# Performance work log

Measured on AMD Instinct MI355X. Metric: run time of the kernel, lower is better.

The kernel has to match this reference:

```python
import jax, jax.numpy as jnp
import numpy as np

B, S, D, H = 2, 2048, 1024, 16
DK = D // H


def setup_inputs() -> dict:
    key = jax.random.key(0)
    ks = jax.random.split(key, 11)
    s = 1.0 / np.sqrt(D)
    inp = {
        "q": jax.random.normal(ks[0], (B, S, D), jnp.float32),
        "k": jax.random.normal(ks[1], (B, S, D), jnp.float32),
        "v": jax.random.normal(ks[2], (B, S, D), jnp.float32),
        # causal (lower-triangular) decoder mask, broadcast over batch & heads
        "mask": jnp.tril(jnp.ones((S, S), jnp.int32))[None, None, :, :],
        "Wq": jax.random.normal(ks[3], (D, D), jnp.float32) * s,
        "bq": jax.random.normal(ks[4], (D,), jnp.float32) * s,
        "Wk": jax.random.normal(ks[5], (D, D), jnp.float32) * s,
        "bk": jax.random.normal(ks[6], (D,), jnp.float32) * s,
        "Wv": jax.random.normal(ks[7], (D, D), jnp.float32) * s,
        "bv": jax.random.normal(ks[8], (D,), jnp.float32) * s,
        "Wo": jax.random.normal(ks[9], (D, D), jnp.float32) * s,
        "bo": jax.random.normal(ks[10], (D,), jnp.float32) * s,
    }
    return inp


def reference(q, k, v, mask, Wq, bq, Wk, bk, Wv, bv, Wo, bo):
    # projections (nn.Linear: x @ W.T + b)
    def proj(x, W, b):
        return (x @ W.T + b).reshape(B, S, H, DK).transpose(0, 2, 1, 3)  # [B,H,S,DK]

    Q = proj(q, Wq, bq)
    K = proj(k, Wk, bk)
    V = proj(v, Wv, bv)

    scores = jnp.einsum("bhsd,bhtd->bhst", Q, K) / jnp.sqrt(jnp.float32(DK))
    scores = jnp.where(mask == 0, jnp.float32(-1e9), scores)
    attn = jax.nn.softmax(scores, axis=-1)  # dropout=0.0 -> identity
    ctx = jnp.einsum("bhst,bhtd->bhsd", attn, V)
    ctx = ctx.transpose(0, 2, 1, 3).reshape(B, S, D)
    return ctx @ Wo.T + bo
```

## Files before the change

### kernel.cpp

```cpp
#include <hip/hip_runtime.h>

typedef __bf16 bf16;
typedef __bf16 bf16x4 __attribute__((ext_vector_type(4)));
typedef __bf16 bf16x8 __attribute__((ext_vector_type(8)));
typedef float floatx4 __attribute__((ext_vector_type(4)));

#define NB 2
#define NS 2048
#define ND 1024
#define NH 16
#define NDK 64
#define NM (NB * NS)

__device__ __forceinline__ void async_cp16(const void* g, void* l) {
  __builtin_amdgcn_global_load_lds(
      (const __attribute__((address_space(1))) void*)g,
      (__attribute__((address_space(3))) void*)l, 16, 0, 0);
}

__device__ __forceinline__ bf16x8 cvt8(const float* p) {
  float4 lo = *(const float4*)p, hi = *(const float4*)(p + 4);
  bf16x8 o;
  o[0] = (bf16)lo.x; o[1] = (bf16)lo.y; o[2] = (bf16)lo.z; o[3] = (bf16)lo.w;
  o[4] = (bf16)hi.x; o[5] = (bf16)hi.y; o[6] = (bf16)hi.z; o[7] = (bf16)hi.w;
  return o;
}

__device__ __forceinline__ void wg_barrier_lds() {
  __asm__ __volatile__("s_waitcnt lgkmcnt(0)" ::: "memory");
  __builtin_amdgcn_s_barrier();
}

__device__ __forceinline__ void tr2(const void* p, bf16x4& lo, bf16x4& hi) {
  asm volatile("ds_read_b64_tr_b16 %0, %2\n\t"
               "ds_read_b64_tr_b16 %1, %2 offset:512"
               : "=&v"(lo), "=&v"(hi)
               : "v"((const __attribute__((address_space(3))) void*)p));
}

__device__ __forceinline__ float fexp2(float x) {
  float r;
  asm("v_exp_f32 %0, %1" : "=v"(r) : "v"(x));
  return r;
}

struct CvtArgs {
  const float* src[8];
  bf16* dst[8];
  int nblk[8];
  int nseg;
};

__global__ __launch_bounds__(256) void cvt_kernel(CvtArgs a) {
  int b = blockIdx.x, seg = 0;
  while (seg < a.nseg - 1 && b >= a.nblk[seg]) { b -= a.nblk[seg]; ++seg; }
  const size_t idx = ((size_t)b * 256 + threadIdx.x) * 8;
  *(bf16x8*)(a.dst[seg] + idx) = cvt8(a.src[seg] + idx);
}

template <int TM, typename TA, typename TC>
__global__ __launch_bounds__(256) void gemm_dma(
    const TA* __restrict__ A0, const TA* __restrict__ A1, const TA* __restrict__ A2,
    const bf16* __restrict__ W0, const bf16* __restrict__ W1, const bf16* __restrict__ W2,
    const float* __restrict__ bias0, const float* __restrict__ bias1, const float* __restrict__ bias2,
    TC* __restrict__ C0, TC* __restrict__ C1, TC* __restrict__ C2)
{
  const int z = blockIdx.z;
  const TA* A = (z == 0) ? A0 : (z == 1) ? A1 : A2;
  const bf16* W = (z == 0) ? W0 : (z == 1) ? W1 : W2;
  const float* bias = (z == 0) ? bias0 : (z == 1) ? bias1 : bias2;
  TC* C = (z == 0) ? C0 : (z == 1) ? C1 : C2;

  __shared__ bf16 At[TM * 32];
  __shared__ bf16 Bt[128 * 32];

  const int tid = threadIdx.x;
  const int wave = tid >> 6, lane = tid & 63;
  const int q4 = lane >> 4, l15 = lane & 15;
  const int m0 = blockIdx.y * TM, n0 = blockIdx.x * 128;
  constexpr int WM = TM / 2;
  constexpr int MI = WM / 16;
  const int wm = (wave >> 1) * WM, wn = (wave & 1) * 64;

  floatx4 acc[MI][4] = {};

  const bf16* Wg = W + (size_t)(n0 + (lane >> 2)) * ND + (lane & 3) * 8;
  const bf16* Ag = nullptr;
  const float* Af = nullptr;
  const int srow = tid >> 2, sk = (tid & 3) * 8;
  if constexpr (sizeof(TA) == 2)
    Ag = (const bf16*)A + (size_t)(m0 + (lane >> 2)) * ND + (lane & 3) * 8;
  else
    Af = (const float*)A + (size_t)(m0 + srow) * ND + sk;

  for (int k0 = 0; k0 < ND; k0 += 32) {
    bf16x8 a0, a1;
    if constexpr (sizeof(TA) == 4) {
      a0 = cvt8(Af + k0);
      if constexpr (TM == 128) a1 = cvt8(Af + (size_t)64 * ND + k0);
    }
    __syncthreads();
#pragma unroll
    for (int c2 = 0; c2 < 2; ++c2) {
      const int c = wave * 2 + c2;
      async_cp16(Wg + (size_t)c * 16 * ND + k0, &Bt[c * 16 * 32]);
    }
    if constexpr (sizeof(TA) == 2) {
#pragma unroll
      for (int c2 = 0; c2 < TM / 64; ++c2) {
        const int c = wave * (TM / 64) + c2;
        async_cp16(Ag + (size_t)c * 16 * ND + k0, &At[c * 16 * 32]);
      }
    } else {
      *(bf16x8*)&At[srow * 32 + sk] = a0;
      if constexpr (TM == 128) *(bf16x8*)&At[(srow + 64) * 32 + sk] = a1;
    }
    __syncthreads();

    bf16x8 af[MI], bfr[4];
#pragma unroll
    for (int i = 0; i < MI; ++i)
      af[i] = *(const bf16x8*)&At[(wm + i * 16 + l15) * 32 + q4 * 8];
#pragma unroll
    for (int j = 0; j < 4; ++j)
      bfr[j] = *(const bf16x8*)&Bt[(wn + j * 16 + l15) * 32 + q4 * 8];
#pragma unroll
    for (int i = 0; i < MI; ++i)
#pragma unroll
      for (int j = 0; j < 4; ++j)
        acc[i][j] = __builtin_amdgcn_mfma_f32_16x16x32_bf16(af[i], bfr[j], acc[i][j], 0, 0, 0);
  }

#pragma unroll
  for (int j = 0; j < 4; ++j) {
    const int col = n0 + wn + j * 16 + l15;
    const float bv = bias[col];
#pragma unroll
    for (int i = 0; i < MI; ++i) {
      const int rowb = m0 + wm + i * 16 + q4 * 4;
#pragma unroll
      for (int r = 0; r < 4; ++r)
        C[(size_t)(rowb + r) * ND + col] = (TC)(acc[i][j][r] + bv);
    }
  }
}

#define NEGBIG (-1e30f)
#define LDP 72

__global__ __launch_bounds__(256) void attn_kernel(
    const bf16* __restrict__ Q, const bf16* __restrict__ K,
    const bf16* __restrict__ V, bf16* __restrict__ O)
{
  __shared__ bf16 vt[2][4096];
  __shared__ bf16 pbuf[4][16 * LDP];

  const int bx = blockIdx.x;
  const int h = blockIdx.y, b = blockIdx.z;
  const int tid = threadIdx.x, wave = tid >> 6, lane = tid & 63;
  const int q4 = lane >> 4, l15 = lane & 15;

  const int koff = l15 * ND + q4 * 8;
  const int sg0 = wave * 8 + (lane >> 3);
  const int sg1 = 32 + sg0;
  const int vs0 = ((sg0 >> 2) << 2) + ((lane & 7) >> 1);
  const int vs1 = ((sg1 >> 2) << 2) + ((lane & 7) >> 1);
  const int vd0 = (sg0 & 3) * 16 + (lane & 1) * 8;
  const int vd1 = (sg1 & 3) * 16 + (lane & 1) * 8;
  const int voff0 = vs0 * ND + vd0;
  const int voff1 = vs1 * ND + vd1;

  const int trb = (lane >> 4) * 512 + l15 * 4;

  bf16x8 qf[2];
  floatx4 oacc[4];
  float psum[4];
  bf16x8 kA[8], kB[8];

  auto ldK = [&](int j, bf16x8 (&kk)[8]) {
    const bf16* ub = K + ((size_t)(b * NS + j * 64)) * ND + h * NDK;
#pragma unroll
    for (int nf = 0; nf < 4; ++nf)
#pragma unroll
      for (int t = 0; t < 2; ++t)
        kk[nf * 2 + t] = *(const bf16x8*)(ub + koff + nf * 16 * ND + t * 32);
  };
  auto stageV = [&](int j, int buf) {
    const bf16* ub = V + ((size_t)(b * NS + j * 64)) * ND + h * NDK;
    async_cp16(ub + voff0, &vt[buf][wave * 512]);
    async_cp16(ub + voff1, &vt[buf][2048 + wave * 512]);
  };

  auto body = [&](int j, int iq, bf16x8 (&kc)[8], bf16x8 (&kn)[8]) {
    const int cur = j & 1;

    floatx4 sf[4];
    __builtin_amdgcn_s_setprio(1);
#pragma unroll
    for (int nf = 0; nf < 4; ++nf) {
      floatx4 s = {0.f, 0.f, 0.f, 0.f};
      s = __builtin_amdgcn_mfma_f32_16x16x32_bf16(qf[0], kc[nf * 2 + 0], s, 0, 0, 0);
      s = __builtin_amdgcn_mfma_f32_16x16x32_bf16(qf[1], kc[nf * 2 + 1], s, 0, 0, 0);
      sf[nf] = s;
    }
    __builtin_amdgcn_s_setprio(0);

    wg_barrier_lds();

    if (j < iq) {
      stageV(j + 1, cur ^ 1);
      asm volatile("" ::: "memory");
      ldK(j + 1, kn);
    }

    if (j == iq) {
#pragma unroll
      for (int nf = 0; nf < 4; ++nf) {
        const int kc2 = nf * 16 + l15;
#pragma unroll
        for (int r = 0; r < 4; ++r)
          if (kc2 > wave * 16 + q4 * 4 + r) sf[nf][r] = NEGBIG;
      }
    }

    bf16x4 vlo[4][2], vhi[4][2];
#pragma unroll
    for (int nf = 0; nf < 4; ++nf)
#pragma unroll
      for (int t = 0; t < 2; ++t)
        tr2(&vt[cur][t * 2048 + nf * 64 + trb], vlo[nf][t], vhi[nf][t]);

#pragma unroll
    for (int nf = 0; nf < 4; ++nf)
#pragma unroll
      for (int r = 0; r < 4; ++r) {
        const float pv = fexp2(sf[nf][r]);
        psum[r] += pv;
        pbuf[wave][(q4 * 4 + r) * LDP + nf * 16 + l15] = (bf16)pv;
      }

    asm volatile("s_waitcnt lgkmcnt(0)" ::: "memory");
    __builtin_amdgcn_sched_barrier(0);

    bf16x8 pa0 = *(const bf16x8*)&pbuf[wave][l15 * LDP + q4 * 8];
    bf16x8 pa1 = *(const bf16x8*)&pbuf[wave][l15 * LDP + 32 + q4 * 8];

    __builtin_amdgcn_s_setprio(1);
#pragma unroll
    for (int nf = 0; nf < 4; ++nf) {
      bf16x8 vb0 = __builtin_shufflevector(vlo[nf][0], vhi[nf][0], 0, 1, 2, 3, 4, 5, 6, 7);
      bf16x8 vb1 = __builtin_shufflevector(vlo[nf][1], vhi[nf][1], 0, 1, 2, 3, 4, 5, 6, 7);
      oacc[nf] = __builtin_amdgcn_mfma_f32_16x16x32_bf16(pa0, vb0, oacc[nf], 0, 0, 0);
      oacc[nf] = __builtin_amdgcn_mfma_f32_16x16x32_bf16(pa1, vb1, oacc[nf], 0, 0, 0);
    }
    __builtin_amdgcn_s_setprio(0);
  };

  for (int ph = 0; ph < 2; ++ph) {
    const int iq = ph ? (31 - bx) : bx;
    __syncthreads();

    const size_t qrow0 = (size_t)(b * NS + iq * 64 + wave * 16 + l15);
#pragma unroll
    for (int t = 0; t < 2; ++t) {
      bf16x8 tmp = *(const bf16x8*)(Q + qrow0 * ND + h * NDK + t * 32 + q4 * 8);
#pragma unroll
      for (int e = 0; e < 8; ++e) qf[t][e] = (bf16)((float)tmp[e] * 0.180336880f);
    }

#pragma unroll
    for (int nf = 0; nf < 4; ++nf) oacc[nf] = floatx4{0.f, 0.f, 0.f, 0.f};
#pragma unroll
    for (int r = 0; r < 4; ++r) psum[r] = 0.f;

    stageV(0, 0);
    asm volatile("" ::: "memory");
    ldK(0, kA);
    for (int j = 0; j <= iq; ++j) {
      if ((j & 1) == 0) body(j, iq, kA, kB);
      else              body(j, iq, kB, kA);
    }

#pragma unroll
    for (int r = 0; r < 4; ++r)
#pragma unroll
      for (int off = 1; off < 16; off <<= 1) psum[r] += __shfl_xor(psum[r], off, 16);

#pragma unroll
    for (int nf = 0; nf < 4; ++nf)
#pragma unroll
      for (int r = 0; r < 4; ++r) {
        const int qrow = iq * 64 + wave * 16 + q4 * 4 + r;
        O[(size_t)(b * NS + qrow) * ND + h * NDK + nf * 16 + l15] =
            (bf16)(oacc[nf][r] / psum[r]);
      }
  }
}

extern "C" void kernel_launch(void* const* d_in, const int* in_sizes, int n_in,
                              void* d_out, int out_size, void* d_ws, size_t ws_size,
                              hipStream_t stream) {
  const float* q  = (const float*)d_in[0];
  const float* k  = (const float*)d_in[1];
  const float* v  = (const float*)d_in[2];
  const float* Wq = (const float*)d_in[4];
  const float* bq = (const float*)d_in[5];
  const float* Wk = (const float*)d_in[6];
  const float* bk = (const float*)d_in[7];
  const float* Wv = (const float*)d_in[8];
  const float* bv = (const float*)d_in[9];
  const float* Wo = (const float*)d_in[10];
  const float* bo = (const float*)d_in[11];
  float* out = (float*)d_out;
  char* w = (char*)d_ws;

  const dim3 attn_grid(NS / 128, NH, NB);

  if (ws_size >= (size_t)56 << 20) {
    bf16* xq = (bf16*)(w);
    bf16* xk = (bf16*)(w + ((size_t)8 << 20));
    bf16* xv = (bf16*)(w + ((size_t)16 << 20));
    bf16* wq = (bf16*)(w + ((size_t)24 << 20));
    bf16* wk = (bf16*)(w + ((size_t)26 << 20));
    bf16* wv = (bf16*)(w + ((size_t)28 << 20));
    bf16* wo = (bf16*)(w + ((size_t)30 << 20));
    bf16* Qb = (bf16*)(w + ((size_t)32 << 20));
    bf16* Kb = (bf16*)(w + ((size_t)40 << 20));
    bf16* Vb = (bf16*)(w + ((size_t)48 << 20));
    bf16* Ob = xq;

    CvtArgs ca{};
    const int b4 = (int)((size_t)NM * ND / 2048);
    const int b1 = (int)((size_t)ND * ND / 2048);
    ca.src[0] = q;  ca.dst[0] = xq; ca.nblk[0] = b4;
    ca.src[1] = k;  ca.dst[1] = xk; ca.nblk[1] = b4;
    ca.src[2] = v;  ca.dst[2] = xv; ca.nblk[2] = b4;
    ca.src[3] = Wq; ca.dst[3] = wq; ca.nblk[3] = b1;
    ca.src[4] = Wk; ca.dst[4] = wk; ca.nblk[4] = b1;
    ca.src[5] = Wv; ca.dst[5] = wv; ca.nblk[5] = b1;
    ca.src[6] = Wo; ca.dst[6] = wo; ca.nblk[6] = b1;
    ca.nseg = 7;
    cvt_kernel<<<3 * b4 + 4 * b1, 256, 0, stream>>>(ca);

    gemm_dma<128, bf16, bf16><<<dim3(8, 32, 3), 256, 0, stream>>>(
        xq, xk, xv, wq, wk, wv, bq, bk, bv, Qb, Kb, Vb);
    attn_kernel<<<attn_grid, 256, 0, stream>>>(Qb, Kb, Vb, Ob);
    gemm_dma<64, bf16, float><<<dim3(8, 64, 1), 256, 0, stream>>>(
        Ob, Ob, Ob, wo, wo, wo, bo, bo, bo, out, out, out);
  } else if (ws_size >= (size_t)40 << 20) {
    bf16* wq = (bf16*)(w);
    bf16* wk = (bf16*)(w + ((size_t)2 << 20));
    bf16* wv = (bf16*)(w + ((size_t)4 << 20));
    bf16* wo = (bf16*)(w + ((size_t)6 << 20));
    bf16* Qb = (bf16*)(w + ((size_t)8 << 20));
    bf16* Kb = (bf16*)(w + ((size_t)16 << 20));
    bf16* Vb = (bf16*)(w + ((size_t)24 << 20));
    bf16* Ob = (bf16*)(w + ((size_t)32 << 20));

    CvtArgs ca{};
    const int b1 = (int)((size_t)ND * ND / 2048);
    ca.src[0] = Wq; ca.dst[0] = wq; ca.nblk[0] = b1;
    ca.src[1] = Wk; ca.dst[1] = wk; ca.nblk[1] = b1;
    ca.src[2] = Wv; ca.dst[2] = wv; ca.nblk[2] = b1;
    ca.src[3] = Wo; ca.dst[3] = wo; ca.nblk[3] = b1;
    ca.nseg = 4;
    cvt_kernel<<<4 * b1, 256, 0, stream>>>(ca);

    gemm_dma<128, float, bf16><<<dim3(8, 32, 3), 256, 0, stream>>>(
        q, k, v, wq, wk, wv, bq, bk, bv, Qb, Kb, Vb);
    attn_kernel<<<attn_grid, 256, 0, stream>>>(Qb, Kb, Vb, Ob);
    gemm_dma<64, bf16, float><<<dim3(8, 64, 1), 256, 0, stream>>>(
        Ob, Ob, Ob, wo, wo, wo, bo, bo, bo, out, out, out);
  }
}
```

Measured before the change: 259.6 us.

## Stage K through swizzled LDS with a triple-buffered async K/V pipeline

K tiles are now loaded with async global-to-LDS copies into an XOR-swizzled shared buffer instead of directly into registers. Both K and V move to a three-stage ring buffer that prefetches two tiles ahead, with a vmcnt wait and a barrier at the top of each iteration. The goal is to hide global load latency better and free the registers that held the double-buffered K fragments. The cost is extra LDS (about 48 KB more), which may lower occupancy, plus an extra LDS read of K on every iteration.

```diff
diff --git a/kernel.cpp b/kernel.cpp
--- a/kernel.cpp
+++ b/kernel.cpp
@@ -24,11 +24,6 @@
   o[0] = (bf16)lo.x; o[1] = (bf16)lo.y; o[2] = (bf16)lo.z; o[3] = (bf16)lo.w;
   o[4] = (bf16)hi.x; o[5] = (bf16)hi.y; o[6] = (bf16)hi.z; o[7] = (bf16)hi.w;
   return o;
-}
-
-__device__ __forceinline__ void wg_barrier_lds() {
-  __asm__ __volatile__("s_waitcnt lgkmcnt(0)" ::: "memory");
-  __builtin_amdgcn_s_barrier();
 }
 
 __device__ __forceinline__ void tr2(const void* p, bf16x4& lo, bf16x4& hi) {
@@ -152,7 +147,8 @@
     const bf16* __restrict__ Q, const bf16* __restrict__ K,
     const bf16* __restrict__ V, bf16* __restrict__ O)
 {
-  __shared__ bf16 vt[2][4096];
+  __shared__ bf16 kt[3][4096];
+  __shared__ bf16 vt[3][4096];
   __shared__ bf16 pbuf[4][16 * LDP];
 
   const int bx = blockIdx.x;
@@ -160,7 +156,9 @@
   const int tid = threadIdx.x, wave = tid >> 6, lane = tid & 63;
   const int q4 = lane >> 4, l15 = lane & 15;
 
-  const int koff = l15 * ND + q4 * 8;
+  const int ksrc = (lane >> 3) * ND + 8 * ((lane & 7) ^ ((lane >> 3) & 7));
+  const int kro0 = l15 * 64 + ((q4 + 0) ^ (l15 & 7)) * 8;
+  const int kro1 = l15 * 64 + ((q4 + 4) ^ (l15 & 7)) * 8;
   const int sg0 = wave * 8 + (lane >> 3);
   const int sg1 = 32 + sg0;
   const int vs0 = ((sg0 >> 2) << 2) + ((lane & 7) >> 1);
@@ -169,30 +167,38 @@
   const int vd1 = (sg1 & 3) * 16 + (lane & 1) * 8;
   const int voff0 = vs0 * ND + vd0;
   const int voff1 = vs1 * ND + vd1;
-
   const int trb = (lane >> 4) * 512 + l15 * 4;
 
   bf16x8 qf[2];
   floatx4 oacc[4];
   float psum[4];
-  bf16x8 kA[8], kB[8];
-
-  auto ldK = [&](int j, bf16x8 (&kk)[8]) {
-    const bf16* ub = K + ((size_t)(b * NS + j * 64)) * ND + h * NDK;
-#pragma unroll
-    for (int nf = 0; nf < 4; ++nf)
-#pragma unroll
-      for (int t = 0; t < 2; ++t)
-        kk[nf * 2 + t] = *(const bf16x8*)(ub + koff + nf * 16 * ND + t * 32);
+
+  auto stage = [&](int j, int buf) {
+    const bf16* ubK = K + ((size_t)(b * NS + j * 64)) * ND + h * NDK;
+    const bf16* ubV = V + ((size_t)(b * NS + j * 64)) * ND + h * NDK;
+#pragma unroll
+    for (int c2 = 0; c2 < 2; ++c2) {
+      const int c = wave * 2 + c2;
+      async_cp16(ubK + c * 8 * ND + ksrc, &kt[buf][c * 512]);
+    }
+    async_cp16(ubV + voff0, &vt[buf][wave * 512]);
+    async_cp16(ubV + voff1, &vt[buf][2048 + wave * 512]);
   };
-  auto stageV = [&](int j, int buf) {
-    const bf16* ub = V + ((size_t)(b * NS + j * 64)) * ND + h * NDK;
-    async_cp16(ub + voff0, &vt[buf][wave * 512]);
-    async_cp16(ub + voff1, &vt[buf][2048 + wave * 512]);
-  };
-
-  auto body = [&](int j, int iq, bf16x8 (&kc)[8], bf16x8 (&kn)[8]) {
-    const int cur = j & 1;
+
+  auto body = [&](int j, int iq, int cur, int tgt) {
+    if (j < iq) asm volatile("s_waitcnt vmcnt(4)" ::: "memory");
+    else        asm volatile("s_waitcnt vmcnt(0)" ::: "memory");
+    __builtin_amdgcn_s_barrier();
+    asm volatile("" ::: "memory");
+
+    if (j + 2 <= iq) stage(j + 2, tgt);
+
+    bf16x8 kc[8];
+#pragma unroll
+    for (int nf = 0; nf < 4; ++nf) {
+      kc[nf * 2 + 0] = *(const bf16x8*)&kt[cur][nf * 1024 + kro0];
+      kc[nf * 2 + 1] = *(const bf16x8*)&kt[cur][nf * 1024 + kro1];
+    }
 
     floatx4 sf[4];
     __builtin_amdgcn_s_setprio(1);
@@ -205,14 +211,6 @@
     }
     __builtin_amdgcn_s_setprio(0);
 
-    wg_barrier_lds();
-
-    if (j < iq) {
-      stageV(j + 1, cur ^ 1);
-      asm volatile("" ::: "memory");
-      ldK(j + 1, kn);
-    }
-
     if (j == iq) {
 #pragma unroll
       for (int nf = 0; nf < 4; ++nf) {
@@ -273,12 +271,13 @@
 #pragma unroll
     for (int r = 0; r < 4; ++r) psum[r] = 0.f;
 
-    stageV(0, 0);
-    asm volatile("" ::: "memory");
-    ldK(0, kA);
+    stage(0, 0);
+    if (iq >= 1) stage(1, 1);
+
+    int jm = 0;
     for (int j = 0; j <= iq; ++j) {
-      if ((j & 1) == 0) body(j, iq, kA, kB);
-      else              body(j, iq, kB, kA);
+      body(j, iq, jm, (jm + 2 >= 3) ? jm - 1 : jm + 2);
+      jm = (jm == 2) ? 0 : jm + 1;
     }
 
 #pragma unroll
```

Result: faster. 233.7 us (-10.0%).
